# Kernel tuning notes

Hardware: AMD Instinct MI355X
Metric: run time of the kernel (lower is better)

The kernel has to match this reference:

```python
import jax, jax.numpy as jnp
import numpy as np

B, T_ENC, H_ENC, H_DEC, ATTN = 64, 4096, 512, 512, 256


def setup_inputs() -> dict:
    key = jax.random.key(0)
    k1, k2, k3, k4, k5 = jax.random.split(key, 5)
    decoder_state = jax.random.normal(k1, (B, H_DEC), dtype=jnp.float32)
    encoder_outputs = jax.random.normal(k2, (B, T_ENC, H_ENC), dtype=jnp.float32)
    # nn.Linear(in, out, bias=False) weight has shape (out, in); apply as x @ W.T
    W_enc = jax.random.normal(k3, (ATTN, H_ENC), dtype=jnp.float32) * (1.0 / np.sqrt(H_ENC))
    W_dec = jax.random.normal(k4, (ATTN, H_DEC), dtype=jnp.float32) * (1.0 / np.sqrt(H_DEC))
    v = jax.random.normal(k5, (1, ATTN), dtype=jnp.float32) * (1.0 / np.sqrt(ATTN))
    return {"decoder_state": decoder_state, "encoder_outputs": encoder_outputs,
            "W_enc": W_enc, "W_dec": W_dec, "v": v}


def reference(decoder_state, encoder_outputs, W_enc, W_dec, v):
    # enc_proj: (B, T, A); dec_proj: (B, 1, A)
    enc_proj = jnp.einsum('bte,ae->bta', encoder_outputs, W_enc)
    dec_proj = jnp.einsum('bd,ad->ba', decoder_state, W_dec)[:, None, :]
    energy = jnp.tanh(enc_proj + dec_proj)              # (B, T, A)
    scores = jnp.einsum('bta,a->bt', energy, v[0])      # (B, T)
    attn_weights = jax.nn.softmax(scores, axis=1)       # (B, T)
    context = jnp.einsum('bte,bt->be', encoder_outputs, attn_weights)  # (B, H_enc)
    return context, attn_weights
```

## Files before the change

kernel.cpp:

```cpp
#include <hip/hip_runtime.h>
#include <hip/hip_bf16.h>

#define B 64
#define T_ENC 4096
#define H_ENC 512
#define H_DEC 512
#define ATTN 256

#define BM 64
#define BK 32
#define LDA 40
#define TC 256

typedef __attribute__((ext_vector_type(8))) short bf16x8;
typedef __attribute__((ext_vector_type(4))) float f32x4;

__device__ __forceinline__ unsigned short f2bf(float f) {
    unsigned int u = __float_as_uint(f);
    unsigned int rounding = 0x7fffu + ((u >> 16) & 1u);
    return (unsigned short)((u + rounding) >> 16);
}

__device__ __forceinline__ float fast_tanh(float x) {
    float ax = fabsf(x);
    float e = __expf(2.0f * fminf(ax, 15.0f));
    float t = 1.0f - 2.0f / (e + 1.0f);
    return copysignf(t, x);
}

__global__ void convw_kernel(const float* __restrict__ W,
                             unsigned short* __restrict__ out) {
    int i = (blockIdx.x * 256 + threadIdx.x) * 4;
    float4 x = *(const float4*)(W + i);
    ushort4 u;
    u.x = f2bf(x.x); u.y = f2bf(x.y); u.z = f2bf(x.z); u.w = f2bf(x.w);
    *(ushort4*)(out + i) = u;
}

__global__ void decproj_kernel(const float* __restrict__ dec,
                               const float* __restrict__ Wdec,
                               float* __restrict__ dproj) {
    __shared__ float sdec[H_DEC];
    int b = blockIdx.x;
    int tid = threadIdx.x;
    sdec[tid]       = dec[b * H_DEC + tid];
    sdec[tid + 256] = dec[b * H_DEC + tid + 256];
    __syncthreads();
    const float* wrow = Wdec + (size_t)tid * H_DEC;
    float acc = 0.0f;
#pragma unroll 4
    for (int k = 0; k < H_DEC; k += 4) {
        float4 w4 = *(const float4*)(wrow + k);
        acc += w4.x * sdec[k] + w4.y * sdec[k + 1] + w4.z * sdec[k + 2] + w4.w * sdec[k + 3];
    }
    dproj[b * ATTN + tid] = acc;
}

__global__ __launch_bounds__(256) void scores_kernel(
    const float* __restrict__ enc,
    const unsigned short* __restrict__ wencb,
    const float* __restrict__ dproj,
    const float* __restrict__ v,
    float* __restrict__ scores)
{
    __shared__ unsigned short Abuf[BM * LDA];
    __shared__ unsigned short Bbuf[ATTN * LDA];
    __shared__ float sPart[BM * 4];

    const int tid  = threadIdx.x;
    const int wave = tid >> 6;
    const int lane = tid & 63;
    const int quad = lane >> 4;
    const int l16  = lane & 15;
    const int m0   = blockIdx.x * BM;
    const int b    = m0 >> 12;

    f32x4 acc[4][4];
#pragma unroll
    for (int mi = 0; mi < 4; ++mi)
#pragma unroll
        for (int ni = 0; ni < 4; ++ni) {
            f32x4 z = {0.0f, 0.0f, 0.0f, 0.0f};
            acc[mi][ni] = z;
        }

    for (int k0 = 0; k0 < H_ENC; k0 += BK) {
#pragma unroll
        for (int rep = 0; rep < 2; ++rep) {
            int idx = rep * 1024 + tid * 4;
            int r = idx >> 5, c = idx & 31;
            float4 x = *(const float4*)(enc + (size_t)(m0 + r) * H_ENC + k0 + c);
            ushort4 u;
            u.x = f2bf(x.x); u.y = f2bf(x.y); u.z = f2bf(x.z); u.w = f2bf(x.w);
            *(ushort4*)(&Abuf[r * LDA + c]) = u;
        }
#pragma unroll
        for (int rep = 0; rep < 4; ++rep) {
            int chunk = rep * 256 + tid;
            int r = chunk >> 2, off = (chunk & 3) * 8;
            bf16x8 x = *(const bf16x8*)(wencb + (size_t)r * H_ENC + k0 + off);
            *(bf16x8*)(&Bbuf[r * LDA + off]) = x;
        }
        __syncthreads();

        bf16x8 afrag[4], bfrag[4];
#pragma unroll
        for (int mi = 0; mi < 4; ++mi)
            afrag[mi] = *(const bf16x8*)(&Abuf[(mi * 16 + l16) * LDA + quad * 8]);
#pragma unroll
        for (int ni = 0; ni < 4; ++ni)
            bfrag[ni] = *(const bf16x8*)(&Bbuf[(wave * 64 + ni * 16 + l16) * LDA + quad * 8]);

#pragma unroll
        for (int mi = 0; mi < 4; ++mi)
#pragma unroll
            for (int ni = 0; ni < 4; ++ni)
                acc[mi][ni] = __builtin_amdgcn_mfma_f32_16x16x32_bf16(
                    afrag[mi], bfrag[ni], acc[mi][ni], 0, 0, 0);
        __syncthreads();
    }

    float decp[4], vv[4];
#pragma unroll
    for (int ni = 0; ni < 4; ++ni) {
        int a = wave * 64 + ni * 16 + l16;
        decp[ni] = dproj[b * ATTN + a];
        vv[ni]   = v[a];
    }
#pragma unroll
    for (int mi = 0; mi < 4; ++mi) {
#pragma unroll
        for (int r = 0; r < 4; ++r) {
            float sum = 0.0f;
#pragma unroll
            for (int ni = 0; ni < 4; ++ni) {
                float x = acc[mi][ni][r] + decp[ni];
                sum += fast_tanh(x) * vv[ni];
            }
            sum += __shfl_xor(sum, 1);
            sum += __shfl_xor(sum, 2);
            sum += __shfl_xor(sum, 4);
            sum += __shfl_xor(sum, 8);
            if (l16 == 0) {
                int m = mi * 16 + quad * 4 + r;
                sPart[m * 4 + wave] = sum;
            }
        }
    }
    __syncthreads();
    if (tid < BM) {
        float s = sPart[tid * 4 + 0] + sPart[tid * 4 + 1] +
                  sPart[tid * 4 + 2] + sPart[tid * 4 + 3];
        scores[m0 + tid] = s;
    }
}

__global__ void softmax_kernel(const float* __restrict__ scores,
                               float* __restrict__ out) {
    __shared__ float redm[4], reds[4];
    int b = blockIdx.x, tid = threadIdx.x;
    int wave = tid >> 6, lane = tid & 63;
    const float* sb = scores + (size_t)b * T_ENC;
    float s[16];
    float m = -1e30f;
#pragma unroll
    for (int i = 0; i < 16; ++i) {
        s[i] = sb[i * 256 + tid];
        m = fmaxf(m, s[i]);
    }
#pragma unroll
    for (int o = 1; o < 64; o <<= 1) m = fmaxf(m, __shfl_xor(m, o));
    if (lane == 0) redm[wave] = m;
    __syncthreads();
    m = fmaxf(fmaxf(redm[0], redm[1]), fmaxf(redm[2], redm[3]));
    float sum = 0.0f;
#pragma unroll
    for (int i = 0; i < 16; ++i) {
        s[i] = __expf(s[i] - m);
        sum += s[i];
    }
#pragma unroll
    for (int o = 1; o < 64; o <<= 1) sum += __shfl_xor(sum, o);
    if (lane == 0) reds[wave] = sum;
    __syncthreads();
    float inv = 1.0f / (reds[0] + reds[1] + reds[2] + reds[3]);
    float* attn = out + B * H_ENC + (size_t)b * T_ENC;
#pragma unroll
    for (int i = 0; i < 16; ++i) attn[i * 256 + tid] = s[i] * inv;
    out[b * H_ENC + tid] = 0.0f;
    out[b * H_ENC + 256 + tid] = 0.0f;
}

__global__ void context_kernel(const float* __restrict__ enc,
                               const float* __restrict__ attnw,
                               float* __restrict__ ctx) {
    __shared__ float w[TC];
    int b = blockIdx.x;
    int t0 = blockIdx.y * TC;
    int tid = threadIdx.x;
    w[tid] = attnw[(size_t)b * T_ENC + t0 + tid];
    __syncthreads();
    int e  = (tid & 127) * 4;
    int tl = tid >> 7;
    const float* base = enc + ((size_t)b * T_ENC + t0 + tl) * H_ENC + e;
    float4 acc = {0.0f, 0.0f, 0.0f, 0.0f};
#pragma unroll 4
    for (int i = 0; i < TC; i += 2) {
        float4 x = *(const float4*)(base + (size_t)i * H_ENC);
        float wt = w[i + tl];
        acc.x += wt * x.x; acc.y += wt * x.y;
        acc.z += wt * x.z; acc.w += wt * x.w;
    }
    float* c = &ctx[b * H_ENC + e];
    atomicAdd(c + 0, acc.x);
    atomicAdd(c + 1, acc.y);
    atomicAdd(c + 2, acc.z);
    atomicAdd(c + 3, acc.w);
}

extern "C" void kernel_launch(void* const* d_in, const int* in_sizes, int n_in,
                              void* d_out, int out_size, void* d_ws, size_t ws_size,
                              hipStream_t stream) {
    const float* dec  = (const float*)d_in[0];
    const float* enc  = (const float*)d_in[1];
    const float* Wenc = (const float*)d_in[2];
    const float* Wdec = (const float*)d_in[3];
    const float* v    = (const float*)d_in[4];
    float* out = (float*)d_out;
    float* ws  = (float*)d_ws;

    float* scores = ws;
    float* dproj  = ws + (size_t)B * T_ENC;
    unsigned short* wencb = (unsigned short*)(ws + (size_t)B * T_ENC + B * ATTN);

    hipLaunchKernelGGL(convw_kernel, dim3((ATTN * H_ENC) / 1024), dim3(256), 0, stream,
                       Wenc, wencb);
    hipLaunchKernelGGL(decproj_kernel, dim3(B), dim3(256), 0, stream, dec, Wdec, dproj);
    hipLaunchKernelGGL(scores_kernel, dim3((B * T_ENC) / BM), dim3(256), 0, stream,
                       enc, wencb, dproj, v, scores);
    hipLaunchKernelGGL(softmax_kernel, dim3(B), dim3(256), 0, stream, scores, out);
    hipLaunchKernelGGL(context_kernel, dim3(B, T_ENC / TC), dim3(256), 0, stream,
                       enc, out + B * H_ENC, out);
}
```

Baseline: 896.1 us.

## Fuse context accumulation into scores kernel with flash-style partial softmax combine

The scores kernel now computes a per-chunk softmax (local max and sum) and immediately accumulates a partial context vector from the 64 encoder rows it just read, which are likely still in cache. A combine kernel merges chunk maxima and sums, rescales the partial contexts and writes the normalized attention weights. This removes the second full pass over the 512 MB encoder tensor, the separate softmax kernel and the atomics. In exchange it adds a partial-context buffer in workspace and extra reads in the combine step.

```diff
diff --git a/kernel.cpp b/kernel.cpp
--- a/kernel.cpp
+++ b/kernel.cpp
@@ -10,7 +10,6 @@
 #define BM 64
 #define BK 32
 #define LDA 40
-#define TC 256
 
 typedef __attribute__((ext_vector_type(8))) short bf16x8;
 typedef __attribute__((ext_vector_type(4))) float f32x4;
@@ -56,23 +55,27 @@
     dproj[b * ATTN + tid] = acc;
 }
 
-__global__ __launch_bounds__(256) void scores_kernel(
+__global__ __launch_bounds__(256) void fused_kernel(
     const float* __restrict__ enc,
     const unsigned short* __restrict__ wencb,
     const float* __restrict__ dproj,
     const float* __restrict__ v,
-    float* __restrict__ scores)
+    float* __restrict__ scores,
+    float* __restrict__ ctxp,
+    float* __restrict__ ml)
 {
     __shared__ unsigned short Abuf[BM * LDA];
     __shared__ unsigned short Bbuf[ATTN * LDA];
     __shared__ float sPart[BM * 4];
+    __shared__ float sP[BM];
 
     const int tid  = threadIdx.x;
     const int wave = tid >> 6;
     const int lane = tid & 63;
     const int quad = lane >> 4;
     const int l16  = lane & 15;
-    const int m0   = blockIdx.x * BM;
+    const int chunk = blockIdx.x;
+    const int m0   = chunk * BM;
     const int b    = m0 >> 12;
 
     f32x4 acc[4][4];
@@ -96,8 +99,8 @@
         }
 #pragma unroll
         for (int rep = 0; rep < 4; ++rep) {
-            int chunk = rep * 256 + tid;
-            int r = chunk >> 2, off = (chunk & 3) * 8;
+            int chnk = rep * 256 + tid;
+            int r = chnk >> 2, off = (chnk & 3) * 8;
             bf16x8 x = *(const bf16x8*)(wencb + (size_t)r * H_ENC + k0 + off);
             *(bf16x8*)(&Bbuf[r * LDA + off]) = x;
         }
@@ -148,74 +151,91 @@
         }
     }
     __syncthreads();
+
     if (tid < BM) {
         float s = sPart[tid * 4 + 0] + sPart[tid * 4 + 1] +
                   sPart[tid * 4 + 2] + sPart[tid * 4 + 3];
         scores[m0 + tid] = s;
-    }
-}
-
-__global__ void softmax_kernel(const float* __restrict__ scores,
-                               float* __restrict__ out) {
-    __shared__ float redm[4], reds[4];
-    int b = blockIdx.x, tid = threadIdx.x;
-    int wave = tid >> 6, lane = tid & 63;
+        float m = s;
+#pragma unroll
+        for (int o = 1; o < 64; o <<= 1) m = fmaxf(m, __shfl_xor(m, o));
+        float p = __expf(s - m);
+        float l = p;
+#pragma unroll
+        for (int o = 1; o < 64; o <<= 1) l += __shfl_xor(l, o);
+        sP[tid] = p;
+        if (tid == 0) {
+            ml[chunk * 2]     = m;
+            ml[chunk * 2 + 1] = l;
+        }
+    }
+    __syncthreads();
+
+    int e0 = tid * 2;
+    const float* ebase = enc + (size_t)m0 * H_ENC + e0;
+    float cx = 0.0f, cy = 0.0f;
+#pragma unroll 4
+    for (int t = 0; t < BM; ++t) {
+        float wt = sP[t];
+        float2 x = *(const float2*)(ebase + (size_t)t * H_ENC);
+        cx += wt * x.x;
+        cy += wt * x.y;
+    }
+    float* cp = ctxp + (size_t)chunk * H_ENC + e0;
+    cp[0] = cx;
+    cp[1] = cy;
+}
+
+__global__ __launch_bounds__(256) void combine_kernel(
+    const float* __restrict__ scores,
+    const float* __restrict__ ctxp,
+    const float* __restrict__ ml,
+    float* __restrict__ out)
+{
+    __shared__ float sc[64];
+    __shared__ float sML[2];
+    const int b = blockIdx.x;
+    const int tid = threadIdx.x;
+    const int nch = T_ENC / BM;
+
+    if (tid < nch) {
+        float m = ml[(b * nch + tid) * 2];
+        float l = ml[(b * nch + tid) * 2 + 1];
+        float M = m;
+#pragma unroll
+        for (int o = 1; o < 64; o <<= 1) M = fmaxf(M, __shfl_xor(M, o));
+        float scale = __expf(m - M);
+        float contrib = l * scale;
+        float L = contrib;
+#pragma unroll
+        for (int o = 1; o < 64; o <<= 1) L += __shfl_xor(L, o);
+        sc[tid] = scale;
+        if (tid == 0) { sML[0] = M; sML[1] = L; }
+    }
+    __syncthreads();
+    const float M = sML[0];
+    const float invL = 1.0f / sML[1];
+
     const float* sb = scores + (size_t)b * T_ENC;
-    float s[16];
-    float m = -1e30f;
+    float* attn = out + B * H_ENC + (size_t)b * T_ENC;
 #pragma unroll
     for (int i = 0; i < 16; ++i) {
-        s[i] = sb[i * 256 + tid];
-        m = fmaxf(m, s[i]);
-    }
-#pragma unroll
-    for (int o = 1; o < 64; o <<= 1) m = fmaxf(m, __shfl_xor(m, o));
-    if (lane == 0) redm[wave] = m;
-    __syncthreads();
-    m = fmaxf(fmaxf(redm[0], redm[1]), fmaxf(redm[2], redm[3]));
-    float sum = 0.0f;
-#pragma unroll
-    for (int i = 0; i < 16; ++i) {
-        s[i] = __expf(s[i] - m);
-        sum += s[i];
-    }
-#pragma unroll
-    for (int o = 1; o < 64; o <<= 1) sum += __shfl_xor(sum, o);
-    if (lane == 0) reds[wave] = sum;
-    __syncthreads();
-    float inv = 1.0f / (reds[0] + reds[1] + reds[2] + reds[3]);
-    float* attn = out + B * H_ENC + (size_t)b * T_ENC;
-#pragma unroll
-    for (int i = 0; i < 16; ++i) attn[i * 256 + tid] = s[i] * inv;
-    out[b * H_ENC + tid] = 0.0f;
-    out[b * H_ENC + 256 + tid] = 0.0f;
-}
-
-__global__ void context_kernel(const float* __restrict__ enc,
-                               const float* __restrict__ attnw,
-                               float* __restrict__ ctx) {
-    __shared__ float w[TC];
-    int b = blockIdx.x;
-    int t0 = blockIdx.y * TC;
-    int tid = threadIdx.x;
-    w[tid] = attnw[(size_t)b * T_ENC + t0 + tid];
-    __syncthreads();
-    int e  = (tid & 127) * 4;
-    int tl = tid >> 7;
-    const float* base = enc + ((size_t)b * T_ENC + t0 + tl) * H_ENC + e;
-    float4 acc = {0.0f, 0.0f, 0.0f, 0.0f};
+        int t = i * 256 + tid;
+        attn[t] = __expf(sb[t] - M) * invL;
+    }
+
+    int e0 = tid * 2;
+    const float* cp = ctxp + ((size_t)b * nch) * H_ENC + e0;
+    float cx = 0.0f, cy = 0.0f;
 #pragma unroll 4
-    for (int i = 0; i < TC; i += 2) {
-        float4 x = *(const float4*)(base + (size_t)i * H_ENC);
-        float wt = w[i + tl];
-        acc.x += wt * x.x; acc.y += wt * x.y;
-        acc.z += wt * x.z; acc.w += wt * x.w;
-    }
-    float* c = &ctx[b * H_ENC + e];
-    atomicAdd(c + 0, acc.x);
-    atomicAdd(c + 1, acc.y);
-    atomicAdd(c + 2, acc.z);
-    atomicAdd(c + 3, acc.w);
+    for (int i = 0; i < nch; ++i) {
+        float s = sc[i];
+        float2 x = *(const float2*)(cp + (size_t)i * H_ENC);
+        cx += s * x.x;
+        cy += s * x.y;
+    }
+    out[b * H_ENC + e0]     = cx * invL;
+    out[b * H_ENC + e0 + 1] = cy * invL;
 }
 
 extern "C" void kernel_launch(void* const* d_in, const int* in_sizes, int n_in,
@@ -229,16 +249,19 @@
     float* out = (float*)d_out;
     float* ws  = (float*)d_ws;
 
+    const int NCHUNK = (B * T_ENC) / BM;
+
     float* scores = ws;
-    float* dproj  = ws + (size_t)B * T_ENC;
-    unsigned short* wencb = (unsigned short*)(ws + (size_t)B * T_ENC + B * ATTN);
+    float* dproj  = scores + (size_t)B * T_ENC;
+    unsigned short* wencb = (unsigned short*)(dproj + B * ATTN);
+    float* ctxp = dproj + B * ATTN + (ATTN * H_ENC) / 2;
+    float* ml   = ctxp + (size_t)NCHUNK * H_ENC;
 
     hipLaunchKernelGGL(convw_kernel, dim3((ATTN * H_ENC) / 1024), dim3(256), 0, stream,
                        Wenc, wencb);
     hipLaunchKernelGGL(decproj_kernel, dim3(B), dim3(256), 0, stream, dec, Wdec, dproj);
-    hipLaunchKernelGGL(scores_kernel, dim3((B * T_ENC) / BM), dim3(256), 0, stream,
-                       enc, wencb, dproj, v, scores);
-    hipLaunchKernelGGL(softmax_kernel, dim3(B), dim3(256), 0, stream, scores, out);
-    hipLaunchKernelGGL(context_kernel, dim3(B, T_ENC / TC), dim3(256), 0, stream,
-                       enc, out + B * H_ENC, out);
-}
+    hipLaunchKernelGGL(fused_kernel, dim3(NCHUNK), dim3(256), 0, stream,
+                       enc, wencb, dproj, v, scores, ctxp, ml);
+    hipLaunchKernelGGL(combine_kernel, dim3(B), dim3(256), 0, stream,
+                       scores, ctxp, ml, out);
+}
```

Result: faster. 875.3 us (-2.3%).
